# Optimization experiments

Hardware: AMD Instinct MI355X
Metric: run time of the kernel (lower is better)

The kernel has to match this reference:

```python
import jax, jax.numpy as jnp
import numpy as np

B, T, C = 4, 2048, 1024
H = 16
HS = C // H          # 64
FF = 4 * C           # 4096
EPS = 1e-5


def layernorm(x, g, b):
    mu = jnp.mean(x, axis=-1, keepdims=True)
    var = jnp.mean(jnp.square(x - mu), axis=-1, keepdims=True)
    return (x - mu) * jax.lax.rsqrt(var + EPS) * g + b


def setup_inputs() -> dict:
    key = jax.random.key(0)
    ks = jax.random.split(key, 16)
    s_in = 1.0 / np.sqrt(C)
    s_ff = 1.0 / np.sqrt(FF)
    return {
        "x": jax.random.normal(ks[0], (B, T, C), jnp.float32),
        # per-head Q/K/V projections stacked: [H, C, HS]
        "Wq": jax.random.normal(ks[1], (H, C, HS), jnp.float32) * s_in,
        "Wk": jax.random.normal(ks[2], (H, C, HS), jnp.float32) * s_in,
        "Wv": jax.random.normal(ks[3], (H, C, HS), jnp.float32) * s_in,
        "Wproj": jax.random.normal(ks[4], (C, C), jnp.float32) * s_in,
        "bproj": jnp.zeros((C,), jnp.float32),
        "W1": jax.random.normal(ks[5], (C, FF), jnp.float32) * s_in,
        "b1": jnp.zeros((FF,), jnp.float32),
        "W2": jax.random.normal(ks[6], (FF, C), jnp.float32) * s_ff,
        "b2": jnp.zeros((C,), jnp.float32),
        "ln1_g": jnp.ones((C,), jnp.float32),
        "ln1_b": jnp.zeros((C,), jnp.float32),
        "ln2_g": jnp.ones((C,), jnp.float32),
        "ln2_b": jnp.zeros((C,), jnp.float32),
    }


def reference(x, Wq, Wk, Wv, Wproj, bproj, W1, b1, W2, b2,
              ln1_g, ln1_b, ln2_g, ln2_b):
    # --- multi-head causal self-attention on layernorm1(x) ---
    h = layernorm(x, ln1_g, ln1_b)                       # [B,T,C]
    q = jnp.einsum('btc,hcd->bhtd', h, Wq)
    k = jnp.einsum('btc,hcd->bhtd', h, Wk)
    v = jnp.einsum('btc,hcd->bhtd', h, Wv)
    scores = jnp.einsum('bhtd,bhsd->bhts', q, k) * (HS ** -0.5)
    causal = jnp.tril(jnp.ones((T, T), bool))
    scores = jnp.where(causal, scores, -jnp.inf)
    att = jax.nn.softmax(scores, axis=-1)                # [B,H,T,T]
    o = jnp.einsum('bhts,bhsd->bthd', att, v).reshape(B, T, C)  # head concat
    x = x + o @ Wproj + bproj
    # --- feedforward on layernorm2(x) ---
    h2 = layernorm(x, ln2_g, ln2_b)
    ff = jax.nn.relu(h2 @ W1 + b1) @ W2 + b2
    return x + ff
```

## Files before the change

kernel.cpp:

```cpp
#include <hip/hip_runtime.h>
#include <cstddef>
#include <cstdio>

#define Bn   4
#define Tn   2048
#define Cn   1024
#define Hn   16
#define HSn  64
#define FFn  4096
#define ROWS (Bn*Tn)
#define QKVW (3*Cn)

typedef __attribute__((ext_vector_type(8))) __bf16 bf16x8;
typedef __attribute__((ext_vector_type(4))) float f32x4;

__device__ __forceinline__ unsigned short f2bf(float f){
  unsigned int u = __float_as_uint(f);
  unsigned int r = (u + 0x7fffu + ((u >> 16) & 1u)) >> 16;
  return (unsigned short)r;
}

#define GLD16(g, l) __builtin_amdgcn_global_load_lds( \
    (__attribute__((address_space(1))) void*)(void*)(g), \
    (__attribute__((address_space(3))) void*)(l), 16, 0, 0)

__device__ __forceinline__ float wave_sum_f(float v){
#pragma unroll
  for (int o = 32; o > 0; o >>= 1) v += __shfl_xor(v, o);
  return v;
}

__global__ void ln_bf16(const float* __restrict__ x, const float* __restrict__ g,
                        const float* __restrict__ bb, unsigned short* __restrict__ y){
  const int row = blockIdx.x;
  const int tid = threadIdx.x;
  const float4 v = reinterpret_cast<const float4*>(x + (size_t)row * Cn)[tid];
  float s  = v.x + v.y + v.z + v.w;
  float ss = v.x*v.x + v.y*v.y + v.z*v.z + v.w*v.w;
  s = wave_sum_f(s); ss = wave_sum_f(ss);
  __shared__ float sm[4], sm2[4];
  const int w = tid >> 6, lane = tid & 63;
  if (lane == 0){ sm[w] = s; sm2[w] = ss; }
  __syncthreads();
  const float tot  = sm[0] + sm[1] + sm[2] + sm[3];
  const float tot2 = sm2[0] + sm2[1] + sm2[2] + sm2[3];
  const float mu = tot * (1.0f / Cn);
  const float rs = rsqrtf(tot2 * (1.0f / Cn) - mu * mu + 1e-5f);
  const float4 gv = reinterpret_cast<const float4*>(g)[tid];
  const float4 bv = reinterpret_cast<const float4*>(bb)[tid];
  ushort4 o;
  o.x = f2bf((v.x - mu) * rs * gv.x + bv.x);
  o.y = f2bf((v.y - mu) * rs * gv.y + bv.y);
  o.z = f2bf((v.z - mu) * rs * gv.z + bv.z);
  o.w = f2bf((v.w - mu) * rs * gv.w + bv.w);
  reinterpret_cast<ushort4*>(y + (size_t)row * Cn)[tid] = o;
}

__global__ void transpose_cast(const float* __restrict__ in, unsigned short* __restrict__ out,
                               int R, int Cc){
  __shared__ float t[64][65];
  const int tid = threadIdx.x;
  const int r0 = blockIdx.y * 64, c0 = blockIdx.x * 64;
  const int rb = tid >> 6, cl = tid & 63;
#pragma unroll
  for (int j = 0; j < 16; ++j)
    t[rb + j*4][cl] = in[(size_t)(r0 + rb + j*4) * Cc + c0 + cl];
  __syncthreads();
#pragma unroll
  for (int j = 0; j < 16; ++j)
    out[(size_t)(c0 + rb + j*4) * R + r0 + cl] = f2bf(t[cl][rb + j*4]);
}

__global__ void repack_qkv_t(const float* __restrict__ Wq, const float* __restrict__ Wk,
                             const float* __restrict__ Wv, unsigned short* __restrict__ Wrt){
  __shared__ float t[64][65];
  const int tid = threadIdx.x;
  const int kb = blockIdx.x * 64;
  const int hh = blockIdx.y;
  const int sec = hh >> 4, h = hh & 15;
  const float* W = (sec == 0) ? Wq : ((sec == 1) ? Wk : Wv);
  const int rb = tid >> 6, dl = tid & 63;
#pragma unroll
  for (int j = 0; j < 16; ++j)
    t[rb + j*4][dl] = W[h * (Cn*HSn) + (size_t)(kb + rb + j*4) * HSn + dl];
  __syncthreads();
#pragma unroll
  for (int j = 0; j < 16; ++j)
    Wrt[(size_t)(sec*Cn + h*64 + rb + j*4) * Cn + kb + dl] = f2bf(t[dl][rb + j*4]);
}

template<int RELU, int OUT_BF16>
__global__ __launch_bounds__(256)
void gemm_mfma(const unsigned short* __restrict__ A, const unsigned short* __restrict__ Bt,
               void* __restrict__ Cout, int M, int N, int K,
               const float* __restrict__ bias, const float* __restrict__ resid){
  __shared__ __align__(16) unsigned short As[128*32];
  __shared__ __align__(16) unsigned short Bs[128*32];
  const int tid = threadIdx.x;
  const int wave = tid >> 6, lane = tid & 63;
  const int wm = wave >> 1, wn = wave & 1;

  const int id = blockIdx.x + gridDim.x * blockIdx.y;
  const int Nbn = gridDim.x;
  const int xcd = id & 7;
  const int sidx = id >> 3;
  const int pm = sidx / Nbn;
  const int bm = xcd + 8 * pm;
  const int bn = sidx - pm * Nbn;

  const int srow = lane >> 2;
  const int row0 = wave*16 + srow;
  const int sw = (((lane & 3) ^ ((row0 >> 1) & 3)) * 8);
  const unsigned short* Ag0 = A  + (size_t)(bm*128 + row0) * K + sw;
  const unsigned short* Bg0 = Bt + (size_t)(bn*128 + row0) * K + sw;
  unsigned short* AsW0 = As + (wave*16) * 32;
  unsigned short* AsW1 = As + (wave*16 + 64) * 32;
  unsigned short* BsW0 = Bs + (wave*16) * 32;
  unsigned short* BsW1 = Bs + (wave*16 + 64) * 32;

  f32x4 acc[4][4] = {};

  const int fr = lane & 15;
  const int Lq = lane >> 4;
  const int fx = ((Lq ^ ((fr >> 1) & 3)) * 8);

  for (int kt = 0; kt < K; kt += 32){
    __syncthreads();
    GLD16(Ag0 + kt,                AsW0);
    GLD16(Ag0 + (size_t)64*K + kt, AsW1);
    GLD16(Bg0 + kt,                BsW0);
    GLD16(Bg0 + (size_t)64*K + kt, BsW1);
    __syncthreads();

    bf16x8 af[4], bfv[4];
#pragma unroll
    for (int mi = 0; mi < 4; ++mi)
      af[mi] = *reinterpret_cast<const bf16x8*>(&As[(wm*64 + mi*16 + fr) * 32 + fx]);
#pragma unroll
    for (int ni = 0; ni < 4; ++ni)
      bfv[ni] = *reinterpret_cast<const bf16x8*>(&Bs[(wn*64 + ni*16 + fr) * 32 + fx]);
#pragma unroll
    for (int mi = 0; mi < 4; ++mi)
#pragma unroll
      for (int ni = 0; ni < 4; ++ni)
        acc[mi][ni] = __builtin_amdgcn_mfma_f32_16x16x32_bf16(
            af[mi], bfv[ni], acc[mi][ni], 0, 0, 0);
  }

  const int lc = lane & 15, lr4 = (lane >> 4) * 4;
#pragma unroll
  for (int ni = 0; ni < 4; ++ni){
    const int col = bn*128 + wn*64 + ni*16 + lc;
    const float bv = bias ? bias[col] : 0.f;
#pragma unroll
    for (int mi = 0; mi < 4; ++mi){
      const int rowb = bm*128 + wm*64 + mi*16 + lr4;
#pragma unroll
      for (int r = 0; r < 4; ++r){
        float v = acc[mi][ni][r] + bv;
        if (RELU) v = fmaxf(v, 0.f);
        if (resid) v += resid[(size_t)(rowb + r) * N + col];
        if (OUT_BF16)
          ((unsigned short*)Cout)[(size_t)(rowb + r) * N + col] = f2bf(v);
        else
          ((float*)Cout)[(size_t)(rowb + r) * N + col] = v;
      }
    }
  }
}

__global__ void blockify_kv(const unsigned short* __restrict__ qkv,
                            unsigned short* __restrict__ Kb,
                            unsigned short* __restrict__ Vb){
  const int st = blockIdx.x, h = blockIdx.y, b = blockIdx.z;
  const int tid = threadIdx.x;
  const size_t base = ((size_t)(b*Hn + h)*32 + st) * 4096;
#pragma unroll
  for (int it = 0; it < 2; ++it){
    const int idx = it*256 + tid;
    const int s = idx >> 3, d8 = idx & 7;
    const uint4 v = *reinterpret_cast<const uint4*>(
        qkv + (size_t)(b*Tn + st*64 + s)*QKVW + Cn + h*64 + d8*8);
    *reinterpret_cast<uint4*>(Kb + base + d8*512 + ((s ^ d8) * 8)) = v;
  }
#pragma unroll
  for (int it = 0; it < 2; ++it){
    const int idx = it*256 + tid;
    const int d = idx & 63, s8 = idx >> 6;
    unsigned short tmp[8];
#pragma unroll
    for (int j = 0; j < 8; ++j)
      tmp[j] = qkv[(size_t)(b*Tn + st*64 + s8*8 + j)*QKVW + 2*Cn + h*64 + d];
    ushort4 lo, hi;
    lo.x = tmp[0]; lo.y = tmp[1]; lo.z = tmp[2]; lo.w = tmp[3];
    hi.x = tmp[4]; hi.y = tmp[5]; hi.z = tmp[6]; hi.w = tmp[7];
    *reinterpret_cast<ushort4*>(Vb + base + s8*512 + ((d ^ s8) * 8))     = lo;
    *reinterpret_cast<ushort4*>(Vb + base + s8*512 + ((d ^ s8) * 8) + 4) = hi;
  }
}

__global__ __launch_bounds__(512, 2)
void attn_mfma3(const unsigned short* __restrict__ qkv,
                const unsigned short* __restrict__ Kb,
                const unsigned short* __restrict__ Vb,
                unsigned short* __restrict__ O){
  __shared__ __align__(16) unsigned short Kls[2][4096];
  __shared__ __align__(16) unsigned short Vls[2][4096];
  __shared__ __align__(16) unsigned short Pt[8][16][72];

  const int bh = blockIdx.x;
  const int b = bh >> 4, h = bh & 15;
  const int pg = blockIdx.y;
  const int tid = threadIdx.x;
  const int wv = tid >> 6, l = tid & 63;
  const int strip = (wv < 4) ? pg : (7 - pg);
  const int qblk = strip*4 + (wv & 3);
  const int Lq = l >> 4, fr = l & 15;
  const int maxst = (7 - pg)*4 + 3;

  const size_t kvbase = ((size_t)(b*Hn + h) * 32) * 4096;

  union U { uint4 u; bf16x8 v; };
  U qf[4][2];
  const unsigned short* Qbase = qkv + ((size_t)(b*Tn + qblk*64)) * QKVW + h*64;
#pragma unroll
  for (int f = 0; f < 4; ++f){
    const unsigned short* qr = Qbase + (size_t)(f*16 + fr) * QKVW + Lq*8;
    qf[f][0].u = *reinterpret_cast<const uint4*>(qr);
    qf[f][1].u = *reinterpret_cast<const uint4*>(qr + 32);
  }

  f32x4 Oa[4][4] = {};
  float lsum[4] = {0.f, 0.f, 0.f, 0.f};
  const float C1 = 0.18033688011112042f;
  const float C2 = 28.853900817779268f;

  auto stage = [&](int st, int buf){
    const unsigned short* gk = Kb + kvbase + (size_t)st*4096 + wv*512 + l*8;
    const unsigned short* gv = Vb + kvbase + (size_t)st*4096 + wv*512 + l*8;
    GLD16(gk, &Kls[buf][wv*512]);
    GLD16(gv, &Vls[buf][wv*512]);
  };

  stage(0, 0);

  for (int st = 0; st <= maxst; ++st){
    const int buf = st & 1;
    __syncthreads();
    if (st < maxst) stage(st + 1, buf ^ 1);
    if (st > qblk) continue;

    U k0[4], k1[4];
#pragma unroll
    for (int sb = 0; sb < 4; ++sb){
      const int s = sb*16 + fr;
      k0[sb].u = *reinterpret_cast<const uint4*>(&Kls[buf][ Lq   *512 + ((s ^  Lq   ) * 8)]);
      k1[sb].u = *reinterpret_cast<const uint4*>(&Kls[buf][(4+Lq)*512 + ((s ^ (4+Lq)) * 8)]);
    }
    U v0[4], v1[4];
#pragma unroll
    for (int db = 0; db < 4; ++db){
      const int d = db*16 + fr;
      v0[db].u = *reinterpret_cast<const uint4*>(&Vls[buf][ Lq   *512 + ((d ^  Lq   ) * 8)]);
      v1[db].u = *reinterpret_cast<const uint4*>(&Vls[buf][(4+Lq)*512 + ((d ^ (4+Lq)) * 8)]);
    }

    const bool diag = (st == qblk);
#pragma unroll
    for (int f = 0; f < 4; ++f){
      f32x4 S[4];
#pragma unroll
      for (int sb = 0; sb < 4; ++sb){
        f32x4 z = {0.f, 0.f, 0.f, 0.f};
        z     = __builtin_amdgcn_mfma_f32_16x16x32_bf16(k0[sb].v, qf[f][0].v, z, 0, 0, 0);
        S[sb] = __builtin_amdgcn_mfma_f32_16x16x32_bf16(k1[sb].v, qf[f][1].v, z, 0, 0, 0);
      }
#pragma unroll
      for (int sb = 0; sb < 4; ++sb){
        float p0 = exp2f(fmaf(S[sb][0], C1, -C2));
        float p1 = exp2f(fmaf(S[sb][1], C1, -C2));
        float p2 = exp2f(fmaf(S[sb][2], C1, -C2));
        float p3 = exp2f(fmaf(S[sb][3], C1, -C2));
        if (diag){
          const int s0 = sb*16 + Lq*4, q = f*16 + fr;
          if (s0 + 0 > q) p0 = 0.f;
          if (s0 + 1 > q) p1 = 0.f;
          if (s0 + 2 > q) p2 = 0.f;
          if (s0 + 3 > q) p3 = 0.f;
        }
        lsum[f] += (p0 + p1) + (p2 + p3);
        const unsigned int pk0 = (unsigned int)f2bf(p0) | ((unsigned int)f2bf(p1) << 16);
        const unsigned int pk1 = (unsigned int)f2bf(p2) | ((unsigned int)f2bf(p3) << 16);
        *reinterpret_cast<uint2*>(&Pt[wv][fr][sb*16 + Lq*4]) = make_uint2(pk0, pk1);
      }
      U pf0, pf1;
      pf0.u = *reinterpret_cast<const uint4*>(&Pt[wv][fr][Lq*8]);
      pf1.u = *reinterpret_cast<const uint4*>(&Pt[wv][fr][32 + Lq*8]);
#pragma unroll
      for (int db = 0; db < 4; ++db){
        Oa[db][f] = __builtin_amdgcn_mfma_f32_16x16x32_bf16(v0[db].v, pf0.v, Oa[db][f], 0, 0, 0);
        Oa[db][f] = __builtin_amdgcn_mfma_f32_16x16x32_bf16(v1[db].v, pf1.v, Oa[db][f], 0, 0, 0);
      }
    }
  }

#pragma unroll
  for (int f = 0; f < 4; ++f){
    float s = lsum[f];
    s += __shfl_xor(s, 16);
    s += __shfl_xor(s, 32);
    const float inv = 1.0f / s;
    const size_t orow = (size_t)(b*Tn + qblk*64 + f*16 + fr);
#pragma unroll
    for (int db = 0; db < 4; ++db){
      ushort4 o;
      o.x = f2bf(Oa[db][f][0] * inv);
      o.y = f2bf(Oa[db][f][1] * inv);
      o.z = f2bf(Oa[db][f][2] * inv);
      o.w = f2bf(Oa[db][f][3] * inv);
      *reinterpret_cast<ushort4*>(&O[orow*Cn + h*64 + db*16 + Lq*4]) = o;
    }
  }
}

extern "C" void kernel_launch(void* const* d_in, const int* in_sizes, int n_in,
                              void* d_out, int out_size, void* d_ws, size_t ws_size,
                              hipStream_t stream){
  const float* x     = (const float*)d_in[0];
  const float* Wq    = (const float*)d_in[1];
  const float* Wk    = (const float*)d_in[2];
  const float* Wv    = (const float*)d_in[3];
  const float* Wproj = (const float*)d_in[4];
  const float* bproj = (const float*)d_in[5];
  const float* W1    = (const float*)d_in[6];
  const float* b1    = (const float*)d_in[7];
  const float* W2    = (const float*)d_in[8];
  const float* b2    = (const float*)d_in[9];
  const float* ln1_g = (const float*)d_in[10];
  const float* ln1_b = (const float*)d_in[11];
  const float* ln2_g = (const float*)d_in[12];
  const float* ln2_b = (const float*)d_in[13];
  float* out = (float*)d_out;

  const size_t MB = 1024ull * 1024ull;
  if (ws_size < 192ull * MB){
    fprintf(stderr, "kernel_launch: need 192MB workspace, got %zu\n", ws_size);
    return;
  }
  char* ws = (char*)d_ws;
  float*          x1    = (float*)(ws + 0);
  unsigned short* h     = (unsigned short*)(ws + 32 * MB);
  unsigned short* qkvb  = (unsigned short*)(ws + 48 * MB);
  unsigned short* ff1   = (unsigned short*)(ws + 48 * MB);
  unsigned short* Kb    = (unsigned short*)(ws + 96 * MB);
  unsigned short* Vb    = (unsigned short*)(ws + 112 * MB);
  unsigned short* Ob    = (unsigned short*)(ws + 128 * MB);
  unsigned short* Wrt   = (unsigned short*)(ws + 144 * MB);
  unsigned short* Wpt   = (unsigned short*)(ws + 150 * MB);
  unsigned short* W1t   = (unsigned short*)(ws + 152 * MB);
  unsigned short* W2t   = (unsigned short*)(ws + 160 * MB);

  repack_qkv_t<<<dim3(Cn/64, 3*Hn), 256, 0, stream>>>(Wq, Wk, Wv, Wrt);
  transpose_cast<<<dim3(Cn/64,  Cn/64),  256, 0, stream>>>(Wproj, Wpt, Cn,  Cn);
  transpose_cast<<<dim3(FFn/64, Cn/64),  256, 0, stream>>>(W1,    W1t, Cn,  FFn);
  transpose_cast<<<dim3(Cn/64,  FFn/64), 256, 0, stream>>>(W2,    W2t, FFn, Cn);

  ln_bf16<<<ROWS, 256, 0, stream>>>(x, ln1_g, ln1_b, h);
  gemm_mfma<0,1><<<dim3(QKVW/128, ROWS/128), 256, 0, stream>>>(
      h, Wrt, qkvb, ROWS, QKVW, Cn, nullptr, nullptr);
  blockify_kv<<<dim3(Tn/64, Hn, Bn), 256, 0, stream>>>(qkvb, Kb, Vb);
  attn_mfma3<<<dim3(64, 4), 512, 0, stream>>>(qkvb, Kb, Vb, Ob);
  gemm_mfma<0,0><<<dim3(Cn/128, ROWS/128), 256, 0, stream>>>(
      Ob, Wpt, x1, ROWS, Cn, Cn, bproj, x);
  ln_bf16<<<ROWS, 256, 0, stream>>>(x1, ln2_g, ln2_b, h);
  gemm_mfma<1,1><<<dim3(FFn/128, ROWS/128), 256, 0, stream>>>(
      h, W1t, ff1, ROWS, FFn, Cn, b1, nullptr);
  gemm_mfma<0,0><<<dim3(Cn/128, ROWS/128), 256, 0, stream>>>(
      ff1, W2t, out, ROWS, Cn, FFn, b2, x1);
}
```

Baseline: 602.4 us.

## Replace GEMM with 256x256-tile, 8-wave kernel using double-buffered async LDS prefetch

Replaces the 128x128 single-buffered GEMM with a 256x256 tile kernel using 8 waves and a K-step of 64. The next K tile is prefetched into a 4-slot LDS ring with global_load_lds, ordered by manual vmcnt/lgkmcnt waits and raw s_barrier. MFMA bursts are wrapped in s_setprio, and block IDs are remapped per XCD for L2 locality. This aims to hide global-load latency and raise arithmetic intensity per block. In exchange it uses more LDS and registers, and launches fewer blocks on the smaller GEMMs (128 for N=1024).

```diff
diff --git a/kernel.cpp b/kernel.cpp
--- a/kernel.cpp
+++ b/kernel.cpp
@@ -90,71 +90,140 @@
 }
 
 template<int RELU, int OUT_BF16>
-__global__ __launch_bounds__(256)
-void gemm_mfma(const unsigned short* __restrict__ A, const unsigned short* __restrict__ Bt,
-               void* __restrict__ Cout, int M, int N, int K,
-               const float* __restrict__ bias, const float* __restrict__ resid){
-  __shared__ __align__(16) unsigned short As[128*32];
-  __shared__ __align__(16) unsigned short Bs[128*32];
-  const int tid = threadIdx.x;
-  const int wave = tid >> 6, lane = tid & 63;
-  const int wm = wave >> 1, wn = wave & 1;
-
-  const int id = blockIdx.x + gridDim.x * blockIdx.y;
+__global__ __launch_bounds__(512, 2)
+void gemm256(const unsigned short* __restrict__ A, const unsigned short* __restrict__ Bt,
+             void* __restrict__ Cout, int M, int N, int K,
+             const float* __restrict__ bias, const float* __restrict__ resid){
+  __shared__ __align__(16) unsigned short As[4 * 8192];
+  __shared__ __align__(16) unsigned short Bs[4 * 8192];
+  const int tid  = threadIdx.x;
+  const int wid  = tid >> 6, lane = tid & 63;
+  const int wm   = wid >> 2, wn = wid & 3;
+  const int fr   = lane & 15, Lq = lane >> 4;
+
+  const int id  = blockIdx.x + gridDim.x * blockIdx.y;
   const int Nbn = gridDim.x;
-  const int xcd = id & 7;
-  const int sidx = id >> 3;
-  const int pm = sidx / Nbn;
-  const int bm = xcd + 8 * pm;
-  const int bn = sidx - pm * Nbn;
-
-  const int srow = lane >> 2;
-  const int row0 = wave*16 + srow;
-  const int sw = (((lane & 3) ^ ((row0 >> 1) & 3)) * 8);
-  const unsigned short* Ag0 = A  + (size_t)(bm*128 + row0) * K + sw;
-  const unsigned short* Bg0 = Bt + (size_t)(bn*128 + row0) * K + sw;
-  unsigned short* AsW0 = As + (wave*16) * 32;
-  unsigned short* AsW1 = As + (wave*16 + 64) * 32;
-  unsigned short* BsW0 = Bs + (wave*16) * 32;
-  unsigned short* BsW1 = Bs + (wave*16 + 64) * 32;
-
-  f32x4 acc[4][4] = {};
-
-  const int fr = lane & 15;
-  const int Lq = lane >> 4;
-  const int fx = ((Lq ^ ((fr >> 1) & 3)) * 8);
-
-  for (int kt = 0; kt < K; kt += 32){
-    __syncthreads();
-    GLD16(Ag0 + kt,                AsW0);
-    GLD16(Ag0 + (size_t)64*K + kt, AsW1);
-    GLD16(Bg0 + kt,                BsW0);
-    GLD16(Bg0 + (size_t)64*K + kt, BsW1);
-    __syncthreads();
-
-    bf16x8 af[4], bfv[4];
-#pragma unroll
-    for (int mi = 0; mi < 4; ++mi)
-      af[mi] = *reinterpret_cast<const bf16x8*>(&As[(wm*64 + mi*16 + fr) * 32 + fx]);
+  const int cpx = (gridDim.x * gridDim.y) >> 3;
+  const int wg  = (id & 7) * cpx + (id >> 3);
+  const int bm  = wg / Nbn;
+  const int bn  = wg - bm * Nbn;
+
+  const int srow  = wid * 8 + (lane >> 3);
+  const int skoff = (((lane & 7) ^ (srow & 7)) * 8);
+  const unsigned short* Abase = A  + (size_t)(bm * 256 + srow) * K + skoff;
+  const unsigned short* Bbase = Bt + (size_t)(bn * 256 + srow) * K + skoff;
+
+  auto stA = [&](int t, int h){
+    const unsigned short* g0 = Abase + (size_t)h * 128 * K + (size_t)t * 64;
+    unsigned short* l0 = As + (((2*t + h) & 3) * 8192) + wid * 512;
+    GLD16(g0, l0);
+    GLD16(g0 + (size_t)64 * K, l0 + 4096);
+  };
+  auto stB = [&](int t, int h){
+    const unsigned short* g0 = Bbase + (size_t)h * 128 * K + (size_t)t * 64;
+    unsigned short* l0 = Bs + (((2*t + h) & 3) * 8192) + wid * 512;
+    GLD16(g0, l0);
+    GLD16(g0 + (size_t)64 * K, l0 + 4096);
+  };
+
+  const int kx0 = (( Lq      ^ (fr & 7)) * 8);
+  const int kx1 = (((4 + Lq) ^ (fr & 7)) * 8);
+
+  f32x4 acc[8][4] = {};
+  const int NT = K >> 6;
+
+  stA(0, 0); stB(0, 0); stA(0, 1); stB(0, 1);
+
+  for (int t = 0; t < NT; ++t){
+    const unsigned short* aS = As + (((2*t + wm) & 3) * 8192);
+    const unsigned short* bS = Bs + (((2*t + (wn >> 1)) & 3) * 8192)
+                                  + ((wn & 1) * 64) * 64;
+    const bool pf = (t + 1 < NT);
+
+    if (pf){ stA(t + 1, 0); stB(t + 1, 0); }
+    if (pf) asm volatile("s_waitcnt vmcnt(4)" ::: "memory");
+    else    asm volatile("s_waitcnt vmcnt(0)" ::: "memory");
+    asm volatile("s_barrier" ::: "memory");
+
+    bf16x8 af[4], bf[4];
+
 #pragma unroll
     for (int ni = 0; ni < 4; ++ni)
-      bfv[ni] = *reinterpret_cast<const bf16x8*>(&Bs[(wn*64 + ni*16 + fr) * 32 + fx]);
-#pragma unroll
-    for (int mi = 0; mi < 4; ++mi)
+      bf[ni] = *reinterpret_cast<const bf16x8*>(&bS[(ni*16 + fr) * 64 + kx0]);
+#pragma unroll
+    for (int m2 = 0; m2 < 4; ++m2)
+      af[m2] = *reinterpret_cast<const bf16x8*>(&aS[(m2*16 + fr) * 64 + kx0]);
+    if (pf) stA(t + 1, 1);
+    asm volatile("s_barrier" ::: "memory");
+    asm volatile("s_waitcnt lgkmcnt(0)" ::: "memory");
+    __builtin_amdgcn_s_setprio(1);
+#pragma unroll
+    for (int m2 = 0; m2 < 4; ++m2)
 #pragma unroll
       for (int ni = 0; ni < 4; ++ni)
-        acc[mi][ni] = __builtin_amdgcn_mfma_f32_16x16x32_bf16(
-            af[mi], bfv[ni], acc[mi][ni], 0, 0, 0);
-  }
-
-  const int lc = lane & 15, lr4 = (lane >> 4) * 4;
+        acc[m2][ni] = __builtin_amdgcn_mfma_f32_16x16x32_bf16(
+            af[m2], bf[ni], acc[m2][ni], 0, 0, 0);
+    __builtin_amdgcn_s_setprio(0);
+    asm volatile("s_barrier" ::: "memory");
+
+#pragma unroll
+    for (int m2 = 0; m2 < 4; ++m2)
+      af[m2] = *reinterpret_cast<const bf16x8*>(&aS[((4+m2)*16 + fr) * 64 + kx0]);
+    if (pf) stB(t + 1, 1);
+    asm volatile("s_barrier" ::: "memory");
+    asm volatile("s_waitcnt lgkmcnt(0)" ::: "memory");
+    __builtin_amdgcn_s_setprio(1);
+#pragma unroll
+    for (int m2 = 0; m2 < 4; ++m2)
+#pragma unroll
+      for (int ni = 0; ni < 4; ++ni)
+        acc[4+m2][ni] = __builtin_amdgcn_mfma_f32_16x16x32_bf16(
+            af[m2], bf[ni], acc[4+m2][ni], 0, 0, 0);
+    __builtin_amdgcn_s_setprio(0);
+    asm volatile("s_barrier" ::: "memory");
+
+#pragma unroll
+    for (int ni = 0; ni < 4; ++ni)
+      bf[ni] = *reinterpret_cast<const bf16x8*>(&bS[(ni*16 + fr) * 64 + kx1]);
+#pragma unroll
+    for (int m2 = 0; m2 < 4; ++m2)
+      af[m2] = *reinterpret_cast<const bf16x8*>(&aS[(m2*16 + fr) * 64 + kx1]);
+    asm volatile("s_barrier" ::: "memory");
+    asm volatile("s_waitcnt lgkmcnt(0)" ::: "memory");
+    __builtin_amdgcn_s_setprio(1);
+#pragma unroll
+    for (int m2 = 0; m2 < 4; ++m2)
+#pragma unroll
+      for (int ni = 0; ni < 4; ++ni)
+        acc[m2][ni] = __builtin_amdgcn_mfma_f32_16x16x32_bf16(
+            af[m2], bf[ni], acc[m2][ni], 0, 0, 0);
+    __builtin_amdgcn_s_setprio(0);
+    asm volatile("s_barrier" ::: "memory");
+
+#pragma unroll
+    for (int m2 = 0; m2 < 4; ++m2)
+      af[m2] = *reinterpret_cast<const bf16x8*>(&aS[((4+m2)*16 + fr) * 64 + kx1]);
+    asm volatile("s_barrier" ::: "memory");
+    asm volatile("s_waitcnt lgkmcnt(0)" ::: "memory");
+    __builtin_amdgcn_s_setprio(1);
+#pragma unroll
+    for (int m2 = 0; m2 < 4; ++m2)
+#pragma unroll
+      for (int ni = 0; ni < 4; ++ni)
+        acc[4+m2][ni] = __builtin_amdgcn_mfma_f32_16x16x32_bf16(
+            af[m2], bf[ni], acc[4+m2][ni], 0, 0, 0);
+    __builtin_amdgcn_s_setprio(0);
+    asm volatile("s_barrier" ::: "memory");
+  }
+
+  const int lc = fr, lr4 = Lq * 4;
 #pragma unroll
   for (int ni = 0; ni < 4; ++ni){
-    const int col = bn*128 + wn*64 + ni*16 + lc;
+    const int col = bn*256 + wn*64 + ni*16 + lc;
     const float bv = bias ? bias[col] : 0.f;
 #pragma unroll
-    for (int mi = 0; mi < 4; ++mi){
-      const int rowb = bm*128 + wm*64 + mi*16 + lr4;
+    for (int mi = 0; mi < 8; ++mi){
+      const int rowb = bm*256 + wm*128 + mi*16 + lr4;
 #pragma unroll
       for (int r = 0; r < 4; ++r){
         float v = acc[mi][ni][r] + bv;
@@ -366,15 +435,15 @@
   transpose_cast<<<dim3(Cn/64,  FFn/64), 256, 0, stream>>>(W2,    W2t, FFn, Cn);
 
   ln_bf16<<<ROWS, 256, 0, stream>>>(x, ln1_g, ln1_b, h);
-  gemm_mfma<0,1><<<dim3(QKVW/128, ROWS/128), 256, 0, stream>>>(
+  gemm256<0,1><<<dim3(QKVW/256, ROWS/256), 512, 0, stream>>>(
       h, Wrt, qkvb, ROWS, QKVW, Cn, nullptr, nullptr);
   blockify_kv<<<dim3(Tn/64, Hn, Bn), 256, 0, stream>>>(qkvb, Kb, Vb);
   attn_mfma3<<<dim3(64, 4), 512, 0, stream>>>(qkvb, Kb, Vb, Ob);
-  gemm_mfma<0,0><<<dim3(Cn/128, ROWS/128), 256, 0, stream>>>(
+  gemm256<0,0><<<dim3(Cn/256, ROWS/256), 512, 0, stream>>>(
       Ob, Wpt, x1, ROWS, Cn, Cn, bproj, x);
   ln_bf16<<<ROWS, 256, 0, stream>>>(x1, ln2_g, ln2_b, h);
-  gemm_mfma<1,1><<<dim3(FFn/128, ROWS/128), 256, 0, stream>>>(
+  gemm256<1,1><<<dim3(FFn/256, ROWS/256), 512, 0, stream>>>(
       h, W1t, ff1, ROWS, FFn, Cn, b1, nullptr);
-  gemm_mfma<0,0><<<dim3(Cn/128, ROWS/128), 256, 0, stream>>>(
+  gemm256<0,0><<<dim3(Cn/256, ROWS/256), 512, 0, stream>>>(
       ff1, W2t, out, ROWS, Cn, FFn, b2, x1);
 }
```

Measured after the change: 656.5 us. +9.0%, slower.

## Add 256x256-tile MFMA GEMM with swizzled LDS and prefetch for QKV and FF1

Applied to the files above, without the earlier changes.

Introduces a 512-thread GEMM kernel computing 256x256 output tiles with a K-step of 64. It uses XOR-swizzled LDS layouts, direct global-to-LDS loads, and a double-buffered prefetch of the next K tile guarded by vmcnt waits. The QKV projection and the first FFN GEMM now use it instead of the 128x128 kernel. The larger tiles raise arithmetic intensity and cut global traffic, at the cost of 128 KB LDS per block, high register pressure, and fewer blocks (384 and 512), which may leave some CUs underused.

```diff
diff --git a/kernel.cpp b/kernel.cpp
--- a/kernel.cpp
+++ b/kernel.cpp
@@ -90,6 +90,112 @@
 }
 
 template<int RELU, int OUT_BF16>
+__global__ __launch_bounds__(512, 2)
+void gemm256(const unsigned short* __restrict__ A, const unsigned short* __restrict__ Bt,
+             void* __restrict__ Cout, int M, int N, int K,
+             const float* __restrict__ bias, const float* __restrict__ resid){
+  __shared__ __align__(16) unsigned short As[4 * 8192];
+  __shared__ __align__(16) unsigned short Bs[4 * 8192];
+  const int tid  = threadIdx.x;
+  const int wid  = tid >> 6, lane = tid & 63;
+  const int wm   = wid >> 2, wn = wid & 3;
+  const int fr   = lane & 15, Lq = lane >> 4;
+
+  const int id  = blockIdx.x + gridDim.x * blockIdx.y;
+  const int Nbn = gridDim.x;
+  const int cpx = (gridDim.x * gridDim.y) >> 3;
+  const int wg  = (id & 7) * cpx + (id >> 3);
+  const int bm  = wg / Nbn;
+  const int bn  = wg - bm * Nbn;
+
+  const int srow  = wid * 8 + (lane >> 3);
+  const int skoff = (((lane & 7) ^ (srow & 7)) * 8);
+  const unsigned short* Abase = A  + (size_t)(bm * 256 + srow) * K + skoff;
+  const unsigned short* Bbase = Bt + (size_t)(bn * 256 + srow) * K + skoff;
+
+  auto stA = [&](int t, int h){
+    const unsigned short* g0 = Abase + (size_t)h * 128 * K + (size_t)t * 64;
+    unsigned short* l0 = As + (((2*t + h) & 3) * 8192) + wid * 512;
+    GLD16(g0, l0);
+    GLD16(g0 + (size_t)64 * K, l0 + 4096);
+  };
+  auto stB = [&](int t, int h){
+    const unsigned short* g0 = Bbase + (size_t)h * 128 * K + (size_t)t * 64;
+    unsigned short* l0 = Bs + (((2*t + h) & 3) * 8192) + wid * 512;
+    GLD16(g0, l0);
+    GLD16(g0 + (size_t)64 * K, l0 + 4096);
+  };
+
+  f32x4 acc[8][4] = {};
+  const int NT = K >> 6;
+
+  stA(0, 0); stA(0, 1); stB(0, 0); stB(0, 1);
+
+  for (int t = 0; t < NT; ++t){
+    const unsigned short* aS = As + (((2*t + wm) & 3) * 8192);
+    const unsigned short* bS = Bs + (((2*t + (wn >> 1)) & 3) * 8192)
+                                  + ((wn & 1) * 64) * 64;
+    const bool pf = (t + 1 < NT);
+
+    if (pf){ stA(t+1, 0); stA(t+1, 1); stB(t+1, 0); stB(t+1, 1); }
+    __builtin_amdgcn_sched_barrier(0);
+    if (pf) asm volatile("s_waitcnt vmcnt(8)");
+    else    asm volatile("s_waitcnt vmcnt(0)");
+    __builtin_amdgcn_s_barrier();
+
+#pragma unroll
+    for (int kk = 0; kk < 2; ++kk){
+      const int kx = (((kk*4) + Lq) ^ (fr & 7)) * 8;
+      bf16x8 bfv[4], af[4];
+#pragma unroll
+      for (int ni = 0; ni < 4; ++ni)
+        bfv[ni] = *reinterpret_cast<const bf16x8*>(&bS[(ni*16 + fr) * 64 + kx]);
+#pragma unroll
+      for (int m2 = 0; m2 < 4; ++m2)
+        af[m2] = *reinterpret_cast<const bf16x8*>(&aS[(m2*16 + fr) * 64 + kx]);
+#pragma unroll
+      for (int m2 = 0; m2 < 4; ++m2)
+#pragma unroll
+        for (int ni = 0; ni < 4; ++ni)
+          acc[m2][ni] = __builtin_amdgcn_mfma_f32_16x16x32_bf16(
+              af[m2], bfv[ni], acc[m2][ni], 0, 0, 0);
+#pragma unroll
+      for (int m2 = 0; m2 < 4; ++m2)
+        af[m2] = *reinterpret_cast<const bf16x8*>(&aS[((4+m2)*16 + fr) * 64 + kx]);
+#pragma unroll
+      for (int m2 = 0; m2 < 4; ++m2)
+#pragma unroll
+        for (int ni = 0; ni < 4; ++ni)
+          acc[4+m2][ni] = __builtin_amdgcn_mfma_f32_16x16x32_bf16(
+              af[m2], bfv[ni], acc[4+m2][ni], 0, 0, 0);
+    }
+    __builtin_amdgcn_sched_barrier(0);
+    __builtin_amdgcn_s_barrier();
+  }
+
+  const int lc = fr, lr4 = Lq * 4;
+#pragma unroll
+  for (int ni = 0; ni < 4; ++ni){
+    const int col = bn*256 + wn*64 + ni*16 + lc;
+    const float bv = bias ? bias[col] : 0.f;
+#pragma unroll
+    for (int mi = 0; mi < 8; ++mi){
+      const int rowb = bm*256 + wm*128 + mi*16 + lr4;
+#pragma unroll
+      for (int r = 0; r < 4; ++r){
+        float v = acc[mi][ni][r] + bv;
+        if (RELU) v = fmaxf(v, 0.f);
+        if (resid) v += resid[(size_t)(rowb + r) * N + col];
+        if (OUT_BF16)
+          ((unsigned short*)Cout)[(size_t)(rowb + r) * N + col] = f2bf(v);
+        else
+          ((float*)Cout)[(size_t)(rowb + r) * N + col] = v;
+      }
+    }
+  }
+}
+
+template<int RELU, int OUT_BF16>
 __global__ __launch_bounds__(256)
 void gemm_mfma(const unsigned short* __restrict__ A, const unsigned short* __restrict__ Bt,
                void* __restrict__ Cout, int M, int N, int K,
@@ -366,14 +472,14 @@
   transpose_cast<<<dim3(Cn/64,  FFn/64), 256, 0, stream>>>(W2,    W2t, FFn, Cn);
 
   ln_bf16<<<ROWS, 256, 0, stream>>>(x, ln1_g, ln1_b, h);
-  gemm_mfma<0,1><<<dim3(QKVW/128, ROWS/128), 256, 0, stream>>>(
+  gemm256<0,1><<<dim3(QKVW/256, ROWS/256), 512, 0, stream>>>(
       h, Wrt, qkvb, ROWS, QKVW, Cn, nullptr, nullptr);
   blockify_kv<<<dim3(Tn/64, Hn, Bn), 256, 0, stream>>>(qkvb, Kb, Vb);
   attn_mfma3<<<dim3(64, 4), 512, 0, stream>>>(qkvb, Kb, Vb, Ob);
   gemm_mfma<0,0><<<dim3(Cn/128, ROWS/128), 256, 0, stream>>>(
       Ob, Wpt, x1, ROWS, Cn, Cn, bproj, x);
   ln_bf16<<<ROWS, 256, 0, stream>>>(x1, ln2_g, ln2_b, h);
-  gemm_mfma<1,1><<<dim3(FFn/128, ROWS/128), 256, 0, stream>>>(
+  gemm256<1,1><<<dim3(FFn/256, ROWS/256), 512, 0, stream>>>(
       h, W1t, ff1, ROWS, FFn, Cn, b1, nullptr);
   gemm_mfma<0,0><<<dim3(Cn/128, ROWS/128), 256, 0, stream>>>(
       ff1, W2t, out, ROWS, Cn, FFn, b2, x1);
```

New measurement: 581.3 us. 1.04x faster.
